# Kernel optimization log

Hardware: AMD Instinct MI355X
Metric: run time of the kernel (lower is better)

Reference implementation:

```python
import jax, jax.numpy as jnp
import numpy as np

EMBED_DIM = 512
HEADS = 8
ATTN_DIM = EMBED_DIM // HEADS
PF_DIM = 2048
B, L = 4, 2048
LN_EPS = 1e-5


def _linear(x, W, b):
    # nn.Linear: x @ W.T + b, W is [out, in]
    return jnp.einsum('bld,od->blo', x, W) + b


def _layer_norm(x, g, b):
    mu = jnp.mean(x, axis=-1, keepdims=True)
    var = jnp.mean(jnp.square(x - mu), axis=-1, keepdims=True)
    return (x - mu) * jax.lax.rsqrt(var + LN_EPS) * g + b


def _qkv(src, Wq, bq, Wk, bk, Wv, bv):
    def split(t):
        Bb, Ll, _ = t.shape
        return t.reshape(Bb, Ll, HEADS, ATTN_DIM).transpose(0, 2, 1, 3)  # [B,H,L,Dh]
    return (split(_linear(src, Wq, bq)),
            split(_linear(src, Wk, bk)),
            split(_linear(src, Wv, bv)))


def _attention(inp, Q, K1, K2, V1, V2, Wo, bo, ln_g, ln_b, W1, b1, W2, b2):
    # non-softmax linear attention: (Q K1^T) V1 + (Q K2^T) V2
    attn = (jnp.einsum('bhqk,bhkd->bhqd', jnp.einsum('bhqd,bhkd->bhqk', Q, K1), V1)
            + jnp.einsum('bhqk,bhkd->bhqd', jnp.einsum('bhqd,bhkd->bhqk', Q, K2), V2))
    Bb = Q.shape[0]
    attn = attn.transpose(0, 2, 1, 3).reshape(Bb, -1, HEADS * ATTN_DIM)  # [B,L,D]
    x = _linear(attn, Wo, bo)
    x = _layer_norm(inp + x, ln_g, ln_b)          # dropout p=0 (eval)
    ff = _linear(jax.nn.relu(_linear(x, W1, b1)), W2, b2)
    x = _layer_norm(x + ff, ln_g, ln_b)
    return x


def setup_inputs() -> dict:
    key = jax.random.key(0)
    ks = jax.random.split(key, 16)
    s = 0.02
    return {
        'question': jax.random.normal(ks[0], (B, L, EMBED_DIM), jnp.float32),
        'query': jax.random.normal(ks[1], (B, L, EMBED_DIM), jnp.float32),
        'Wq': jax.random.normal(ks[2], (EMBED_DIM, EMBED_DIM), jnp.float32) * s,
        'bq': jnp.zeros((EMBED_DIM,), jnp.float32),
        'Wk': jax.random.normal(ks[3], (EMBED_DIM, EMBED_DIM), jnp.float32) * s,
        'bk': jnp.zeros((EMBED_DIM,), jnp.float32),
        'Wv': jax.random.normal(ks[4], (EMBED_DIM, EMBED_DIM), jnp.float32) * s,
        'bv': jnp.zeros((EMBED_DIM,), jnp.float32),
        'Wo': jax.random.normal(ks[5], (EMBED_DIM, EMBED_DIM), jnp.float32) * s,
        'bo': jnp.zeros((EMBED_DIM,), jnp.float32),
        'ln_g': jnp.ones((EMBED_DIM,), jnp.float32),
        'ln_b': jnp.zeros((EMBED_DIM,), jnp.float32),
        'W1': jax.random.normal(ks[6], (PF_DIM, EMBED_DIM), jnp.float32) * s,
        'b1': jnp.zeros((PF_DIM,), jnp.float32),
        'W2': jax.random.normal(ks[7], (EMBED_DIM, PF_DIM), jnp.float32) * s,
        'b2': jnp.zeros((EMBED_DIM,), jnp.float32),
    }


def reference(question, query, Wq, bq, Wk, bk, Wv, bv, Wo, bo, ln_g, ln_b, W1, b1, W2, b2):
    Q1, K1, V1 = _qkv(question, Wq, bq, Wk, bk, Wv, bv)
    Q2, K2, V2 = _qkv(query, Wq, bq, Wk, bk, Wv, bv)
    question_attn = _attention(question, Q1, K1, K2, V1, V2, Wo, bo, ln_g, ln_b, W1, b1, W2, b2)
    query_attn = _attention(query, Q2, K2, K1, V2, V1, Wo, bo, ln_g, ln_b, W1, b1, W2, b2)
    return jnp.concatenate([question_attn, query_attn], axis=-1)
```

## Files before the change

kernel.cpp:

```cpp
#include <hip/hip_runtime.h>
#include <stdint.h>


#define Bq 4
#define Lq 2048
#define Dq 512
#define PFq 2048
#define Mrows 16384
#define MiBu 1048576ull
#define NSLICE 16

typedef __attribute__((ext_vector_type(8))) short frag_ab;
typedef __attribute__((ext_vector_type(4))) float frag_cd;
typedef __attribute__((ext_vector_type(8))) unsigned short ushort8v;

__device__ __forceinline__ unsigned short f2b(float f) {
    union { float f; uint32_t u; } x; x.f = f;
    uint32_t r = x.u + 0x7fffu + ((x.u >> 16) & 1u);
    return (unsigned short)(r >> 16);
}
__device__ __forceinline__ float b2f(unsigned short u) {
    union { uint32_t u; float f; } x; x.u = ((uint32_t)u) << 16;
    return x.f;
}

#define GLD16(g, l)                                                              \
    __builtin_amdgcn_global_load_lds(                                            \
        (const __attribute__((address_space(1))) void*)(const void*)(g),         \
        (__attribute__((address_space(3))) void*)(void*)(l), 16, 0, 0)

__global__ __launch_bounds__(256) void gemm_bf16(
    const unsigned short* __restrict__ A, const unsigned short* __restrict__ Wt,
    const float* __restrict__ bias, unsigned short* __restrict__ outB,
    int M, int N, int K, int relu)
{
    __shared__ __align__(16) unsigned short Sh[2 * 128 * 64];
    unsigned short* At = Sh;
    unsigned short* Bt = Sh + 128 * 64;
    const int tid = threadIdx.x;
    const int lane = tid & 63;
    const int w = tid >> 6;
    const int wm = (w >> 1) * 64, wn = (w & 1) * 64;
    const int lr = lane & 15;
    const int quad = lane >> 4;
    const size_t bm = (size_t)blockIdx.x * 128, bn = (size_t)blockIdx.y * 128;

    frag_cd acc[4][4] = {};

    const int ar = tid >> 3;
    const int acs = (((tid & 7) ^ (ar & 7)) << 3);
    const unsigned short* Ag = A  + (bm + ar) * (size_t)K + acs;
    const unsigned short* Bg = Wt + (bn + ar) * (size_t)K + acs;
    unsigned short* Asd = At + w * 512;
    unsigned short* Bsd = Bt + w * 512;

    for (int k0 = 0; k0 < K; k0 += 64) {
        __syncthreads();
#pragma unroll
        for (int i = 0; i < 4; ++i) {
            GLD16(Ag + (size_t)(32 * i) * K + k0, Asd + i * 2048);
            GLD16(Bg + (size_t)(32 * i) * K + k0, Bsd + i * 2048);
        }
        __syncthreads();
#pragma unroll
        for (int kk = 0; kk < 2; ++kk) {
            frag_ab a[4], b[4];
#pragma unroll
            for (int i = 0; i < 4; ++i)
                a[i] = *(const frag_ab*)&At[(wm + i * 16 + lr) * 64 +
                                            ((((kk << 2) | quad) ^ (lr & 7)) << 3)];
#pragma unroll
            for (int j = 0; j < 4; ++j)
                b[j] = *(const frag_ab*)&Bt[(wn + j * 16 + lr) * 64 +
                                            ((((kk << 2) | quad) ^ (lr & 7)) << 3)];
#pragma unroll
            for (int i = 0; i < 4; ++i)
#pragma unroll
                for (int j = 0; j < 4; ++j)
                    acc[i][j] = __builtin_amdgcn_mfma_f32_16x16x32_bf16(a[i], b[j], acc[i][j], 0, 0, 0);
        }
    }

    __syncthreads();
    unsigned short* Cs = Sh + w * 4096;
#pragma unroll
    for (int j = 0; j < 4; ++j) {
        const float bv = bias[(int)bn + wn + j * 16 + lr];
#pragma unroll
        for (int i = 0; i < 4; ++i)
#pragma unroll
            for (int r = 0; r < 4; ++r) {
                float v = acc[i][j][r] + bv;
                if (relu) v = fmaxf(v, 0.f);
                Cs[(i * 16 + quad * 4 + r) * 64 + j * 16 + lr] = f2b(v);
            }
    }
    const int rl = lane >> 3;
    const int c8 = (lane & 7) * 8;
#pragma unroll
    for (int k = 0; k < 8; ++k) {
        const int row = rl + k * 8;
        ushort8v val = *(const ushort8v*)&Cs[row * 64 + c8];
        *(ushort8v*)(outB + (size_t)(bm + wm + row) * N + bn + wn + c8) = val;
    }
}

__global__ __launch_bounds__(256) void gemm_res(
    const unsigned short* __restrict__ A, const unsigned short* __restrict__ Wt,
    const float* __restrict__ bias,
    const float* __restrict__ resA, const float* __restrict__ resB,
    unsigned short* __restrict__ outB, int M, int N, int K)
{
    __shared__ __align__(16) unsigned short Sh[128 * 64 + 64 * 64];
    unsigned short* At = Sh;
    unsigned short* Bt = Sh + 128 * 64;
    const int tid = threadIdx.x;
    const int lane = tid & 63;
    const int w = tid >> 6;
    const int wm = w * 32;
    const int lr = lane & 15;
    const int quad = lane >> 4;
    const size_t bm = (size_t)blockIdx.x * 128, bn = (size_t)blockIdx.y * 64;

    frag_cd acc[2][4] = {};

    const int ar = tid >> 3;
    const int acs = (((tid & 7) ^ (ar & 7)) << 3);
    const unsigned short* Ag = A  + (bm + ar) * (size_t)K + acs;
    const unsigned short* Bg = Wt + (bn + ar) * (size_t)K + acs;
    unsigned short* Asd = At + w * 512;
    unsigned short* Bsd = Bt + w * 512;

    for (int k0 = 0; k0 < K; k0 += 64) {
        __syncthreads();
#pragma unroll
        for (int i = 0; i < 4; ++i)
            GLD16(Ag + (size_t)(32 * i) * K + k0, Asd + i * 2048);
#pragma unroll
        for (int i = 0; i < 2; ++i)
            GLD16(Bg + (size_t)(32 * i) * K + k0, Bsd + i * 2048);
        __syncthreads();
#pragma unroll
        for (int kk = 0; kk < 2; ++kk) {
            frag_ab a[2], b[4];
#pragma unroll
            for (int i = 0; i < 2; ++i)
                a[i] = *(const frag_ab*)&At[(wm + i * 16 + lr) * 64 +
                                            ((((kk << 2) | quad) ^ (lr & 7)) << 3)];
#pragma unroll
            for (int j = 0; j < 4; ++j)
                b[j] = *(const frag_ab*)&Bt[(j * 16 + lr) * 64 +
                                            ((((kk << 2) | quad) ^ (lr & 7)) << 3)];
#pragma unroll
            for (int i = 0; i < 2; ++i)
#pragma unroll
                for (int j = 0; j < 4; ++j)
                    acc[i][j] = __builtin_amdgcn_mfma_f32_16x16x32_bf16(a[i], b[j], acc[i][j], 0, 0, 0);
        }
    }

    __syncthreads();
    unsigned short* Cs = Sh + w * 2048;
#pragma unroll
    for (int j = 0; j < 4; ++j) {
        const float bv = bias[(int)bn + j * 16 + lr];
#pragma unroll
        for (int i = 0; i < 2; ++i)
#pragma unroll
            for (int r = 0; r < 4; ++r)
                Cs[(i * 16 + quad * 4 + r) * 64 + j * 16 + lr] = f2b(acc[i][j][r] + bv);
    }
    const int rl = lane >> 3;
    const int c8 = (lane & 7) * 8;
#pragma unroll
    for (int k = 0; k < 4; ++k) {
        const int row = rl + k * 8;
        const int grow = (int)bm + wm + row;
        const size_t idx = (size_t)grow * N + bn + c8;
        ushort8v val = *(const ushort8v*)&Cs[row * 64 + c8];
        float vv[8];
#pragma unroll
        for (int t = 0; t < 8; ++t) vv[t] = b2f(val[t]);
        if (resA) {
            const float* rp = (grow < 8192) ? resA + idx : resB + idx - (size_t)8192 * N;
            float4 ra = *(const float4*)(rp);
            float4 rb = *(const float4*)(rp + 4);
            vv[0] += ra.x; vv[1] += ra.y; vv[2] += ra.z; vv[3] += ra.w;
            vv[4] += rb.x; vv[5] += rb.y; vv[6] += rb.z; vv[7] += rb.w;
        } else {
            ushort8v old = *(const ushort8v*)(outB + idx);
#pragma unroll
            for (int t = 0; t < 8; ++t) vv[t] += b2f(old[t]);
        }
        ushort8v o;
#pragma unroll
        for (int t = 0; t < 8; ++t) o[t] = f2b(vv[t]);
        *(ushort8v*)(outB + idx) = o;
    }
}

__global__ __launch_bounds__(256) void convert_all(
    const float* __restrict__ Wq, const float* __restrict__ Wk,
    const float* __restrict__ Wv, const float* __restrict__ Wo,
    const float* __restrict__ W1, const float* __restrict__ W2,
    const float* __restrict__ question, const float* __restrict__ query,
    const float* __restrict__ bqp, const float* __restrict__ bkp,
    const float* __restrict__ bvp,
    unsigned short* __restrict__ Wqkvb, unsigned short* __restrict__ Wob,
    unsigned short* __restrict__ W1b, unsigned short* __restrict__ W2b,
    unsigned short* __restrict__ Xb, float* __restrict__ bqkv)
{
    const int b = blockIdx.x;
    const float* src; unsigned short* dst; size_t off;
    if (b < 256)        { src = Wq; dst = Wqkvb;          off = (size_t)b * 1024; }
    else if (b < 512)   { src = Wk; dst = Wqkvb + 262144; off = (size_t)(b - 256) * 1024; }
    else if (b < 768)   { src = Wv; dst = Wqkvb + 524288; off = (size_t)(b - 512) * 1024; }
    else if (b < 1024)  { src = Wo; dst = Wob;            off = (size_t)(b - 768) * 1024; }
    else if (b < 2048)  { src = W1; dst = W1b;            off = (size_t)(b - 1024) * 1024; }
    else if (b < 3072)  { src = W2; dst = W2b;            off = (size_t)(b - 2048) * 1024; }
    else if (b < 7168)  { src = question; dst = Xb;       off = (size_t)(b - 3072) * 1024; }
    else if (b < 11264) { src = query; dst = Xb + 4194304; off = (size_t)(b - 7168) * 1024; }
    else {
        const int n = (b - 11264) * 256 + threadIdx.x;
        bqkv[n] = (n < 512) ? bqp[n] : (n < 1024) ? bkp[n - 512] : bvp[n - 1024];
        return;
    }
    const size_t idx = off + threadIdx.x * 4;
    float4 v = *(const float4*)(src + idx);
    ushort4 o;
    o.x = f2b(v.x); o.y = f2b(v.y); o.z = f2b(v.z); o.w = f2b(v.w);
    *(ushort4*)(dst + idx) = o;
}

__global__ __launch_bounds__(256) void s_kernel(
    const unsigned short* __restrict__ QKV, float* __restrict__ Spart)
{
    const int bh = blockIdx.x;
    const int sl = blockIdx.y;
    const int b = bh >> 3, h = bh & 7;
    const int pass = sl >> 3;
    const int l0 = (sl & 7) * 256;
    __shared__ float Ks[64][64];
    __shared__ float Vs[64][64];
    const int tid = threadIdx.x;
    const int tx = tid & 15, ty = tid >> 4;
    const int srow = tid >> 3;
    const int scol = (tid & 7) * 8;
    const size_t rowbase = (size_t)pass * 8192 + (size_t)b * Lq + l0;

    float acc[4][4] = {};

    for (int t0 = 0; t0 < 256; t0 += 64) {
        const unsigned short* kp0 = QKV + (rowbase + t0 + srow) * 1536 + 512 + h * 64 + scol;
        const unsigned short* kp1 = kp0 + (size_t)32 * 1536;
        ushort8v k0 = *(const ushort8v*)kp0;
        ushort8v v0 = *(const ushort8v*)(kp0 + 512);
        ushort8v k1 = *(const ushort8v*)kp1;
        ushort8v v1 = *(const ushort8v*)(kp1 + 512);
        __syncthreads();
#pragma unroll
        for (int e = 0; e < 8; ++e) {
            Ks[srow][scol + e]      = b2f(k0[e]);
            Vs[srow][scol + e]      = b2f(v0[e]);
            Ks[srow + 32][scol + e] = b2f(k1[e]);
            Vs[srow + 32][scol + e] = b2f(v1[e]);
        }
        __syncthreads();
#pragma unroll 4
        for (int rr = 0; rr < 64; ++rr) {
            const float4 kf = *(const float4*)&Ks[rr][ty * 4];
            const float4 vf = *(const float4*)&Vs[rr][tx * 4];
            acc[0][0] = fmaf(kf.x, vf.x, acc[0][0]);
            acc[0][1] = fmaf(kf.x, vf.y, acc[0][1]);
            acc[0][2] = fmaf(kf.x, vf.z, acc[0][2]);
            acc[0][3] = fmaf(kf.x, vf.w, acc[0][3]);
            acc[1][0] = fmaf(kf.y, vf.x, acc[1][0]);
            acc[1][1] = fmaf(kf.y, vf.y, acc[1][1]);
            acc[1][2] = fmaf(kf.y, vf.z, acc[1][2]);
            acc[1][3] = fmaf(kf.y, vf.w, acc[1][3]);
            acc[2][0] = fmaf(kf.z, vf.x, acc[2][0]);
            acc[2][1] = fmaf(kf.z, vf.y, acc[2][1]);
            acc[2][2] = fmaf(kf.z, vf.z, acc[2][2]);
            acc[2][3] = fmaf(kf.z, vf.w, acc[2][3]);
            acc[3][0] = fmaf(kf.w, vf.x, acc[3][0]);
            acc[3][1] = fmaf(kf.w, vf.y, acc[3][1]);
            acc[3][2] = fmaf(kf.w, vf.z, acc[3][2]);
            acc[3][3] = fmaf(kf.w, vf.w, acc[3][3]);
        }
    }

    float* Sp = Spart + ((size_t)bh * NSLICE + sl) * 4096;
#pragma unroll
    for (int i = 0; i < 4; ++i) {
        float4 o = make_float4(acc[i][0], acc[i][1], acc[i][2], acc[i][3]);
        *(float4*)(Sp + (ty * 4 + i) * 64 + tx * 4) = o;
    }
}

__global__ __launch_bounds__(256) void sbt_convert(
    const float* __restrict__ Spart, unsigned short* __restrict__ Sbt)
{
    const int bh = blockIdx.x;
    const int uo = blockIdx.y;
    const float* Sp = Spart + (size_t)bh * (NSLICE * 4096);
    unsigned short* Dp = Sbt + (size_t)bh * 4096;
    const int t = threadIdx.x;
#pragma unroll
    for (int u = 0; u < 4; ++u) {
        const int d = (uo * 4 + u) * 256 + t;
        float v = 0.f;
#pragma unroll
        for (int s = 0; s < NSLICE; ++s) v += Sp[(size_t)s * 4096 + d];
        const int row = d >> 6, col = d & 63;
        Dp[(row >> 5) * 2048 + col * 32 + (row & 31)] = f2b(v);
    }
}

__global__ __launch_bounds__(256) void attn_mfma(
    const unsigned short* __restrict__ QKV, const unsigned short* __restrict__ Sbt,
    unsigned short* __restrict__ Ob)
{
    __shared__ __align__(16) unsigned short Sh[2 * 128 * 32 + 2 * 64 * 32];
    unsigned short* At = Sh;
    unsigned short* Bt = Sh + 2 * 128 * 32;
    const int h = blockIdx.x;
    const int rbase = blockIdx.y * 128;
    const int b = (rbase >> 11) & 3;
    const int bh = b * 8 + h;
    const int tid = threadIdx.x;
    const int lane = tid & 63;
    const int w = tid >> 6;
    const int lr = lane & 15;
    const int quad = lane >> 4;

    {
        const int rloc = tid >> 2, c8 = (tid & 3) * 8;
#pragma unroll
        for (int it = 0; it < 4; ++it) {
            const int kk = it & 1, rh = it >> 1;
            const unsigned short* g = QKV +
                ((size_t)rbase + rh * 64 + rloc) * 1536 + h * 64 + kk * 32 + c8;
            GLD16(g, At + kk * 4096 + rh * 2048 + w * 512);
        }
        const unsigned short* Sg = Sbt + (size_t)bh * 4096 + tid * 8;
#pragma unroll
        for (int bi = 0; bi < 2; ++bi)
            GLD16(Sg + bi * 2048, Bt + bi * 2048 + w * 512);
    }
    __syncthreads();

    frag_cd acc[2][4] = {};
#pragma unroll
    for (int kk = 0; kk < 2; ++kk) {
        frag_ab a[2], bfr[4];
#pragma unroll
        for (int i = 0; i < 2; ++i)
            a[i] = *(const frag_ab*)&At[kk * 4096 + (w * 32 + i * 16 + lr) * 32 + quad * 8];
#pragma unroll
        for (int j = 0; j < 4; ++j)
            bfr[j] = *(const frag_ab*)&Bt[kk * 2048 + (j * 16 + lr) * 32 + quad * 8];
#pragma unroll
        for (int i = 0; i < 2; ++i)
#pragma unroll
            for (int j = 0; j < 4; ++j)
                acc[i][j] = __builtin_amdgcn_mfma_f32_16x16x32_bf16(a[i], bfr[j], acc[i][j], 0, 0, 0);
    }

    __syncthreads();
    unsigned short* Cs = Sh + w * 2048;
#pragma unroll
    for (int i = 0; i < 2; ++i)
#pragma unroll
        for (int j = 0; j < 4; ++j)
#pragma unroll
            for (int r = 0; r < 4; ++r)
                Cs[(i * 16 + quad * 4 + r) * 64 + j * 16 + lr] = f2b(acc[i][j][r]);
    const int rl = lane >> 3;
    const int c8o = (lane & 7) * 8;
#pragma unroll
    for (int k = 0; k < 4; ++k) {
        const int row = rl + k * 8;
        ushort8v val = *(const ushort8v*)&Cs[row * 64 + c8o];
        *(ushort8v*)(Ob + (size_t)(rbase + w * 32 + row) * 512 + h * 64 + c8o) = val;
    }
}

__global__ __launch_bounds__(256) void ln_b16_inplace(
    unsigned short* __restrict__ Y, const float* __restrict__ g,
    const float* __restrict__ bta)
{
    __shared__ float part[8];
    const int row = blockIdx.x;
    const int t = threadIdx.x;
    const int w = t >> 6;
    unsigned short* yr = Y + (size_t)row * Dq;
    const float v0 = b2f(yr[t]), v1 = b2f(yr[t + 256]);
    float s = v0 + v1;
#pragma unroll
    for (int off = 32; off; off >>= 1) s += __shfl_xor(s, off, 64);
    if ((t & 63) == 0) part[w] = s;
    __syncthreads();
    const float mean = (part[0] + part[1] + part[2] + part[3]) * (1.f / Dq);
    const float d0 = v0 - mean, d1 = v1 - mean;
    float q = d0 * d0 + d1 * d1;
#pragma unroll
    for (int off = 32; off; off >>= 1) q += __shfl_xor(q, off, 64);
    if ((t & 63) == 0) part[4 + w] = q;
    __syncthreads();
    const float rstd = rsqrtf((part[4] + part[5] + part[6] + part[7]) * (1.f / Dq) + 1e-5f);
    yr[t] = f2b(d0 * rstd * g[t] + bta[t]);
    yr[t + 256] = f2b(d1 * rstd * g[t + 256] + bta[t + 256]);
}

__global__ __launch_bounds__(256) void ln_b16_out(
    const unsigned short* __restrict__ Y, const float* __restrict__ g,
    const float* __restrict__ bta, float* __restrict__ out)
{
    __shared__ float part[8];
    const int row = blockIdx.x;
    const int t = threadIdx.x;
    const int w = t >> 6;
    const unsigned short* yr = Y + (size_t)row * Dq;
    const float v0 = b2f(yr[t]), v1 = b2f(yr[t + 256]);
    float s = v0 + v1;
#pragma unroll
    for (int off = 32; off; off >>= 1) s += __shfl_xor(s, off, 64);
    if ((t & 63) == 0) part[w] = s;
    __syncthreads();
    const float mean = (part[0] + part[1] + part[2] + part[3]) * (1.f / Dq);
    const float d0 = v0 - mean, d1 = v1 - mean;
    float q = d0 * d0 + d1 * d1;
#pragma unroll
    for (int off = 32; off; off >>= 1) q += __shfl_xor(q, off, 64);
    if ((t & 63) == 0) part[4 + w] = q;
    __syncthreads();
    const float rstd = rsqrtf((part[4] + part[5] + part[6] + part[7]) * (1.f / Dq) + 1e-5f);
    const int half = row >> 13, br = row & 8191;
    float* orow = out + (size_t)br * 1024 + half * 512;
    orow[t] = d0 * rstd * g[t] + bta[t];
    orow[t + 256] = d1 * rstd * g[t + 256] + bta[t + 256];
}

extern "C" void kernel_launch(void* const* d_in, const int* in_sizes, int n_in,
                              void* d_out, int out_size, void* d_ws, size_t ws_size,
                              hipStream_t stream)
{
    const float* question = (const float*)d_in[0];
    const float* query    = (const float*)d_in[1];
    const float* Wq = (const float*)d_in[2];  const float* bqp = (const float*)d_in[3];
    const float* Wk = (const float*)d_in[4];  const float* bkp = (const float*)d_in[5];
    const float* Wv = (const float*)d_in[6];  const float* bvp = (const float*)d_in[7];
    const float* Wo = (const float*)d_in[8];  const float* bo  = (const float*)d_in[9];
    const float* ln_g = (const float*)d_in[10]; const float* ln_b = (const float*)d_in[11];
    const float* W1 = (const float*)d_in[12]; const float* b1 = (const float*)d_in[13];
    const float* W2 = (const float*)d_in[14]; const float* b2 = (const float*)d_in[15];
    float* out = (float*)d_out;
    char* ws = (char*)d_ws;

    unsigned short* QKVb  = (unsigned short*)(ws);
    unsigned short* attnb = (unsigned short*)(ws + 48 * MiBu);
    float* Spart          = (float*)(ws + 48 * MiBu);
    unsigned short* Xb    = (unsigned short*)(ws + 64 * MiBu);
    unsigned short* xbuf  = (unsigned short*)(ws + 64 * MiBu);
    unsigned short* hb    = (unsigned short*)(ws);
    char* wp = ws + 80 * MiBu + 524288;
    unsigned short* Wqkvb = (unsigned short*)wp;  wp += 1536 * 512 * 2;
    unsigned short* Wob   = (unsigned short*)wp;  wp += 512 * 512 * 2;
    unsigned short* W1b   = (unsigned short*)wp;  wp += 2048 * 512 * 2;
    unsigned short* W2b   = (unsigned short*)wp;  wp += 512 * 2048 * 2;
    unsigned short* Sbt   = (unsigned short*)wp;  wp += 32 * 4096 * 2;
    float* bqkv           = (float*)wp;

    dim3 blk(256);

    convert_all<<<11270, blk, 0, stream>>>(Wq, Wk, Wv, Wo, W1, W2, question, query,
                                           bqp, bkp, bvp,
                                           Wqkvb, Wob, W1b, W2b, Xb, bqkv);

    gemm_bf16<<<dim3(128, 12), blk, 0, stream>>>(Xb, Wqkvb, bqkv, QKVb,
                                                 Mrows, 1536, 512, 0);

    s_kernel<<<dim3(32, NSLICE), blk, 0, stream>>>(QKVb, Spart);
    sbt_convert<<<dim3(32, 4), blk, 0, stream>>>(Spart, Sbt);
    attn_mfma<<<dim3(8, 128), blk, 0, stream>>>(QKVb, Sbt, attnb);

    gemm_res<<<dim3(128, 8), blk, 0, stream>>>(attnb, Wob, bo, question, query,
                                               xbuf, Mrows, 512, 512);

    ln_b16_inplace<<<Mrows, blk, 0, stream>>>(xbuf, ln_g, ln_b);

    gemm_bf16<<<dim3(128, 16), blk, 0, stream>>>(xbuf, W1b, b1, hb,
                                                 Mrows, PFq, 512, 1);

    gemm_res<<<dim3(128, 8), blk, 0, stream>>>(hb, W2b, b2, nullptr, nullptr,
                                               xbuf, Mrows, 512, PFq);

    ln_b16_out<<<Mrows, blk, 0, stream>>>(xbuf, ln_g, ln_b, out);
}
```

Before: 330.5 us.

## Replace 128x128 GEMM with 256x256 double-buffered pipelined GEMM for QKV and FFN1

Replaces the 128x128-tile bf16 GEMM with a 512-thread, 256x256-tile kernel specialised for K=512. It double-buffers LDS with global_load_lds staging interleaved into eight MFMA phases, and uses explicit barriers, waitcnts and setprio. A remapped block index groups tiles for L2 locality. The intent is to hide global load latency behind MFMA work and raise data reuse per tile, at the cost of 128KB of LDS, heavier register use and hardcoded K and grid assumptions.

```diff
diff --git a/kernel.cpp b/kernel.cpp
--- a/kernel.cpp
+++ b/kernel.cpp
@@ -29,76 +29,128 @@
         (const __attribute__((address_space(1))) void*)(const void*)(g),         \
         (__attribute__((address_space(3))) void*)(void*)(l), 16, 0, 0)
 
-__global__ __launch_bounds__(256) void gemm_bf16(
+
+#define STG(BUFOFS, REGOFS, GB, ROWOFS, TILE)                                    \
+    { GLD16((GB) + (size_t)(ROWOFS) * 512 + (TILE) * 64,                         \
+            Sh + (BUFOFS) + (REGOFS) + ld);                                      \
+      GLD16((GB) + ((size_t)(ROWOFS) + 64) * 512 + (TILE) * 64,                  \
+            Sh + (BUFOFS) + (REGOFS) + ld + 4096); }
+
+#define VMW(N) asm volatile("s_waitcnt vmcnt(" #N ")" ::: "memory")
+
+#define PHASE(CB, M0, LOADB, STAGE_STMT, WAIT_STMT)                              \
+    {                                                                            \
+        frag_ab a00 = *(const frag_ab*)&Sh[(CB) + (wm + (M0)*16 + lr) * 64 + xo0];      \
+        frag_ab a01 = *(const frag_ab*)&Sh[(CB) + (wm + (M0)*16 + lr) * 64 + xo1];      \
+        frag_ab a10 = *(const frag_ab*)&Sh[(CB) + (wm + (M0)*16 + 16 + lr) * 64 + xo0]; \
+        frag_ab a11 = *(const frag_ab*)&Sh[(CB) + (wm + (M0)*16 + 16 + lr) * 64 + xo1]; \
+        if (LOADB) {                                                             \
+            _Pragma("unroll")                                                    \
+            for (int j = 0; j < 4; ++j) {                                        \
+                bf[j][0] = *(const frag_ab*)&Sh[(CB) + 16384 + (wn + j*16 + lr)*64 + xo0]; \
+                bf[j][1] = *(const frag_ab*)&Sh[(CB) + 16384 + (wn + j*16 + lr)*64 + xo1]; \
+            }                                                                    \
+        }                                                                        \
+        STAGE_STMT;                                                              \
+        WAIT_STMT;                                                               \
+        __builtin_amdgcn_sched_barrier(0);                                       \
+        __builtin_amdgcn_s_barrier();                                            \
+        asm volatile("s_waitcnt lgkmcnt(0)" ::: "memory");                       \
+        __builtin_amdgcn_sched_barrier(0);                                       \
+        __builtin_amdgcn_s_setprio(1);                                           \
+        _Pragma("unroll")                                                        \
+        for (int j = 0; j < 4; ++j) {                                            \
+            acc[(M0)][j]   = __builtin_amdgcn_mfma_f32_16x16x32_bf16(a00, bf[j][0], acc[(M0)][j], 0,0,0);   \
+            acc[(M0)][j]   = __builtin_amdgcn_mfma_f32_16x16x32_bf16(a01, bf[j][1], acc[(M0)][j], 0,0,0);   \
+            acc[(M0)+1][j] = __builtin_amdgcn_mfma_f32_16x16x32_bf16(a10, bf[j][0], acc[(M0)+1][j], 0,0,0); \
+            acc[(M0)+1][j] = __builtin_amdgcn_mfma_f32_16x16x32_bf16(a11, bf[j][1], acc[(M0)+1][j], 0,0,0); \
+        }                                                                        \
+        __builtin_amdgcn_s_setprio(0);                                           \
+        __builtin_amdgcn_sched_barrier(0);                                       \
+        __builtin_amdgcn_s_barrier();                                            \
+        __builtin_amdgcn_sched_barrier(0);                                       \
+    }
+
+__global__ __launch_bounds__(512, 2) void gemm_256(
     const unsigned short* __restrict__ A, const unsigned short* __restrict__ Wt,
     const float* __restrict__ bias, unsigned short* __restrict__ outB,
-    int M, int N, int K, int relu)
-{
-    __shared__ __align__(16) unsigned short Sh[2 * 128 * 64];
-    unsigned short* At = Sh;
-    unsigned short* Bt = Sh + 128 * 64;
+    int M, int N, int relu)
+{
+    __shared__ __align__(16) unsigned short Sh[65536];
     const int tid = threadIdx.x;
     const int lane = tid & 63;
     const int w = tid >> 6;
-    const int wm = (w >> 1) * 64, wn = (w & 1) * 64;
+    const int wm = (w >> 2) * 128;
+    const int wn = (w & 3) * 64;
     const int lr = lane & 15;
     const int quad = lane >> 4;
-    const size_t bm = (size_t)blockIdx.x * 128, bn = (size_t)blockIdx.y * 128;
-
-    frag_cd acc[4][4] = {};
+    const int xo0 = ((quad ^ (lr & 7)) << 3);
+    const int xo1 = (((4 | quad) ^ (lr & 7)) << 3);
+
+    const int nwg = gridDim.x;
+    const int b0 = blockIdx.x;
+    const int bid = (b0 & 7) * (nwg >> 3) + (b0 >> 3);
+    const int mb = M >> 8;
+    const size_t bm = (size_t)(bid % mb) * 256;
+    const size_t bn = (size_t)(bid / mb) * 256;
 
     const int ar = tid >> 3;
-    const int acs = (((tid & 7) ^ (ar & 7)) << 3);
-    const unsigned short* Ag = A  + (bm + ar) * (size_t)K + acs;
-    const unsigned short* Bg = Wt + (bn + ar) * (size_t)K + acs;
-    unsigned short* Asd = At + w * 512;
-    unsigned short* Bsd = Bt + w * 512;
-
-    for (int k0 = 0; k0 < K; k0 += 64) {
-        __syncthreads();
-#pragma unroll
-        for (int i = 0; i < 4; ++i) {
-            GLD16(Ag + (size_t)(32 * i) * K + k0, Asd + i * 2048);
-            GLD16(Bg + (size_t)(32 * i) * K + k0, Bsd + i * 2048);
-        }
-        __syncthreads();
-#pragma unroll
-        for (int kk = 0; kk < 2; ++kk) {
-            frag_ab a[4], b[4];
-#pragma unroll
-            for (int i = 0; i < 4; ++i)
-                a[i] = *(const frag_ab*)&At[(wm + i * 16 + lr) * 64 +
-                                            ((((kk << 2) | quad) ^ (lr & 7)) << 3)];
-#pragma unroll
-            for (int j = 0; j < 4; ++j)
-                b[j] = *(const frag_ab*)&Bt[(wn + j * 16 + lr) * 64 +
-                                            ((((kk << 2) | quad) ^ (lr & 7)) << 3)];
-#pragma unroll
-            for (int i = 0; i < 4; ++i)
-#pragma unroll
-                for (int j = 0; j < 4; ++j)
-                    acc[i][j] = __builtin_amdgcn_mfma_f32_16x16x32_bf16(a[i], b[j], acc[i][j], 0, 0, 0);
-        }
-    }
-
-    __syncthreads();
-    unsigned short* Cs = Sh + w * 4096;
-#pragma unroll
-    for (int j = 0; j < 4; ++j) {
-        const float bv = bias[(int)bn + wn + j * 16 + lr];
-#pragma unroll
-        for (int i = 0; i < 4; ++i)
+    const int sw = ((tid & 7) ^ (ar & 7)) << 3;
+    const unsigned short* Ag = A  + (bm + ar) * (size_t)512 + sw;
+    const unsigned short* Bg = Wt + (bn + ar) * (size_t)512 + sw;
+    const int ld = tid * 8;
+
+    frag_cd acc[8][4] = {};
+    frag_ab bf[4][2];
+
+    STG(0,     16384, Bg, 0,   0);
+    STG(0,     24576, Bg, 128, 0);
+    STG(0,     0,     Ag, 0,   0);
+    STG(0,     8192,  Ag, 128, 0);
+    STG(32768, 16384, Bg, 0,   1);
+    STG(32768, 24576, Bg, 128, 1);
+    VMW(4);
+    __builtin_amdgcn_sched_barrier(0);
+    __builtin_amdgcn_s_barrier();
+    __builtin_amdgcn_sched_barrier(0);
+
+    for (int I = 0; I < 3; ++I) {
+        const int tb = 2 * I + 1, tc = 2 * I + 2, td = 2 * I + 3;
+        PHASE(0,     0, 1, STG(32768, 0,     Ag, 0,   tb), (void)0);
+        PHASE(0,     2, 0, STG(32768, 8192,  Ag, 128, tb), (void)0);
+        PHASE(0,     4, 0, STG(0,     16384, Bg, 0,   tc), (void)0);
+        PHASE(0,     6, 0, STG(0,     24576, Bg, 128, tc), VMW(4));
+        PHASE(32768, 0, 1, STG(0,     0,     Ag, 0,   tc), (void)0);
+        PHASE(32768, 2, 0, STG(0,     8192,  Ag, 128, tc), (void)0);
+        PHASE(32768, 4, 0, STG(32768, 16384, Bg, 0,   td), (void)0);
+        PHASE(32768, 6, 0, STG(32768, 24576, Bg, 128, td), VMW(4));
+    }
+    PHASE(0,     0, 1, STG(32768, 0,    Ag, 0,   7), (void)0);
+    PHASE(0,     2, 0, STG(32768, 8192, Ag, 128, 7), (void)0);
+    PHASE(0,     4, 0, (void)0, (void)0);
+    PHASE(0,     6, 0, (void)0, VMW(0));
+    PHASE(32768, 0, 1, (void)0, (void)0);
+    PHASE(32768, 2, 0, (void)0, (void)0);
+    PHASE(32768, 4, 0, (void)0, (void)0);
+    PHASE(32768, 6, 0, (void)0, (void)0);
+
+    float bv[4];
+#pragma unroll
+    for (int j = 0; j < 4; ++j) bv[j] = bias[(int)bn + wn + j * 16 + lr];
+    unsigned short* Cs = Sh + w * 8192;
+#pragma unroll
+    for (int m = 0; m < 8; ++m)
+#pragma unroll
+        for (int j = 0; j < 4; ++j)
 #pragma unroll
             for (int r = 0; r < 4; ++r) {
-                float v = acc[i][j][r] + bv;
+                float v = acc[m][j][r] + bv[j];
                 if (relu) v = fmaxf(v, 0.f);
-                Cs[(i * 16 + quad * 4 + r) * 64 + j * 16 + lr] = f2b(v);
+                Cs[(m * 16 + quad * 4 + r) * 64 + j * 16 + lr] = f2b(v);
             }
-    }
-    const int rl = lane >> 3;
-    const int c8 = (lane & 7) * 8;
-#pragma unroll
-    for (int k = 0; k < 8; ++k) {
+    const int rl = lane >> 3, c8 = (lane & 7) * 8;
+#pragma unroll
+    for (int k = 0; k < 16; ++k) {
         const int row = rl + k * 8;
         ushort8v val = *(const ushort8v*)&Cs[row * 64 + c8];
         *(ushort8v*)(outB + (size_t)(bm + wm + row) * N + bn + wn + c8) = val;
@@ -477,8 +529,8 @@
                                            bqp, bkp, bvp,
                                            Wqkvb, Wob, W1b, W2b, Xb, bqkv);
 
-    gemm_bf16<<<dim3(128, 12), blk, 0, stream>>>(Xb, Wqkvb, bqkv, QKVb,
-                                                 Mrows, 1536, 512, 0);
+    gemm_256<<<dim3(384), dim3(512), 0, stream>>>(Xb, Wqkvb, bqkv, QKVb,
+                                                  Mrows, 1536, 0);
 
     s_kernel<<<dim3(32, NSLICE), blk, 0, stream>>>(QKVb, Spart);
     sbt_convert<<<dim3(32, 4), blk, 0, stream>>>(Spart, Sbt);
@@ -489,8 +541,8 @@
 
     ln_b16_inplace<<<Mrows, blk, 0, stream>>>(xbuf, ln_g, ln_b);
 
-    gemm_bf16<<<dim3(128, 16), blk, 0, stream>>>(xbuf, W1b, b1, hb,
-                                                 Mrows, PFq, 512, 1);
+    gemm_256<<<dim3(512), dim3(512), 0, stream>>>(xbuf, W1b, b1, hb,
+                                                  Mrows, PFq, 1);
 
     gemm_res<<<dim3(128, 8), blk, 0, stream>>>(hb, W2b, b2, nullptr, nullptr,
                                                xbuf, Mrows, 512, PFq);
```

Measured after the change: 319.9 us. 3.2% less time.
